# Kernel tuning notes

Hardware: AMD Instinct MI355X
Metric: run time of the kernel (lower is better)

## Reference

```python
import jax, jax.numpy as jnp
import numpy as np

STATE_DIM = 64
MEASURE_DIM = 32
N = 1048576  # measurement batch (broadcast column dim of z)


def setup_inputs() -> dict:
    key = jax.random.key(0)
    kz, kf = jax.random.split(key)
    z = jax.random.normal(kz, (MEASURE_DIM, N), dtype=jnp.float32)
    # Parameters initialized as in AKF.__init__ (identity matrices), with a
    # small perturbation on F so the dynamics are non-trivial but S stays
    # well-conditioned for the inverse.
    F = jnp.eye(STATE_DIM, dtype=jnp.float32) + 0.01 * jax.random.normal(kf, (STATE_DIM, STATE_DIM), dtype=jnp.float32)
    H = jnp.eye(MEASURE_DIM, STATE_DIM, dtype=jnp.float32)
    Q = jnp.eye(STATE_DIM, dtype=jnp.float32)
    R = jnp.eye(MEASURE_DIM, dtype=jnp.float32)
    P = jnp.eye(STATE_DIM, dtype=jnp.float32)
    x = jnp.zeros((STATE_DIM, 1), dtype=jnp.float32)
    return {"z": z, "F": F, "H": H, "Q": Q, "R": R, "P": P, "x": x}


def reference(z, F, H, Q, R, P, x):
    # One Kalman filter update step (predict + correct), batched over N
    # measurement columns in z. Returns the updated state estimate, matching
    # the torch module's `return self.x`.
    x_pred = F @ x                      # [s, 1]
    P_pred = F @ P @ F.T + Q            # [s, s]
    y = z - H @ x_pred                  # [m, N] (broadcast of [m,1])
    S = H @ P_pred @ H.T + R            # [m, m]
    K = P_pred @ H.T @ jnp.linalg.inv(S)  # [s, m]
    x_new = x_pred + K @ y              # [s, N]
    return x_new
```

## Files before the change

### kernel.cpp

```cpp
#include <hip/hip_runtime.h>

#define SD 64
#define MD 32

typedef float f32x4 __attribute__((ext_vector_type(4)));
typedef float f32x2 __attribute__((ext_vector_type(2)));

__device__ float g_Kb[SD * MD + SD];

__global__ __launch_bounds__(1024) void akf_prepare(
    const float* __restrict__ F, const float* __restrict__ H,
    const float* __restrict__ Q, const float* __restrict__ R,
    const float* __restrict__ P, const float* __restrict__ x)
{
    __shared__ __align__(16) float sF [SD * SD];
    __shared__ __align__(16) float sFt[SD * 68];
    __shared__ __align__(16) float sP [SD * SD];
    __shared__ __align__(16) float sT [SD * 68];
    __shared__ __align__(16) float sPp[SD * 68];
    __shared__ __align__(16) float sH [MD * SD];
    __shared__ __align__(16) float sHt[SD * 36];
    __shared__ __align__(16) float sA [SD * 36];
    __shared__ __align__(16) float sS [MD * 33];
    __shared__ __align__(16) float sSi[MD * 36];
    __shared__ __align__(16) float sK [SD * 36];
    __shared__ float sx[SD], sxp[SD], sHx[MD];

    const int tid = threadIdx.x;

    for (int idx = tid; idx < SD * SD; idx += 1024) {
        float f = F[idx], p = P[idx];
        int i = idx >> 6, j = idx & 63;
        sF[idx] = f;
        sFt[j * 68 + i] = f;
        sP[idx] = p;
    }
    for (int idx = tid; idx < MD * SD; idx += 1024) {
        float h = H[idx];
        int j = idx >> 6, k = idx & 63;
        sH[idx] = h;
        sHt[k * 36 + j] = h;
    }
    if (tid < SD) sx[tid] = x[tid];
    __syncthreads();

    if (tid < SD) {
        float a = 0.f;
        for (int k = 0; k < SD; ++k) a = fmaf(sFt[k * 68 + tid], sx[k], a);
        sxp[tid] = a;
    }

    {
        const int i = tid >> 4, j0 = (tid & 15) * 4;
        f32x4 acc = {0.f, 0.f, 0.f, 0.f};
        for (int k = 0; k < SD; ++k) {
            const float f = sF[i * 64 + k];
            const f32x4 p4 = *(const f32x4*)&sP[k * 64 + j0];
            acc.x = fmaf(f, p4.x, acc.x);
            acc.y = fmaf(f, p4.y, acc.y);
            acc.z = fmaf(f, p4.z, acc.z);
            acc.w = fmaf(f, p4.w, acc.w);
        }
        *(f32x4*)&sT[i * 68 + j0] = acc;
    }
    __syncthreads();

    {
        const int i = tid >> 4, j0 = (tid & 15) * 4;
        f32x4 acc = *(const f32x4*)&Q[i * 64 + j0];
        for (int k = 0; k < SD; ++k) {
            const float t = sT[i * 68 + k];
            const f32x4 f4 = *(const f32x4*)&sFt[k * 68 + j0];
            acc.x = fmaf(t, f4.x, acc.x);
            acc.y = fmaf(t, f4.y, acc.y);
            acc.z = fmaf(t, f4.z, acc.z);
            acc.w = fmaf(t, f4.w, acc.w);
        }
        *(f32x4*)&sPp[i * 68 + j0] = acc;
    }
    __syncthreads();

    if (tid < MD) {
        float a = 0.f;
        for (int k = 0; k < SD; ++k) a = fmaf(sHt[k * 36 + tid], sxp[k], a);
        sHx[tid] = a;
    }
    if (tid < 512) {
        const int i = tid >> 3, j0 = (tid & 7) * 4;
        f32x4 acc = {0.f, 0.f, 0.f, 0.f};
        for (int k = 0; k < SD; ++k) {
            const float p = sPp[i * 68 + k];
            const f32x4 h4 = *(const f32x4*)&sHt[k * 36 + j0];
            acc.x = fmaf(p, h4.x, acc.x);
            acc.y = fmaf(p, h4.y, acc.y);
            acc.z = fmaf(p, h4.z, acc.z);
            acc.w = fmaf(p, h4.w, acc.w);
        }
        *(f32x4*)&sA[i * 36 + j0] = acc;
    }
    __syncthreads();

    {
        const int i = tid >> 5, j = tid & 31;
        float a = R[i * 32 + j];
        for (int k = 0; k < SD; ++k) a = fmaf(sH[i * 64 + k], sA[k * 36 + j], a);
        sS[i * 33 + j] = a;
    }
    __syncthreads();

    if (tid < 64) {
        float col[MD];
#pragma unroll
        for (int i = 0; i < MD; ++i)
            col[i] = (tid < MD) ? sS[i * 33 + tid] : ((i == tid - MD) ? 1.f : 0.f);
#pragma unroll
        for (int kp = 0; kp < MD; ++kp) {
            const float piv = __shfl(col[kp], kp);
            const float r = 1.0f / piv;
            col[kp] *= r;
            const float pr = col[kp];
#pragma unroll
            for (int i = 0; i < MD; ++i) {
                if (i == kp) continue;
                const float f = __shfl(col[i], kp);
                col[i] = fmaf(-f, pr, col[i]);
            }
        }
        if (tid >= MD) {
            const int j = tid - MD;
#pragma unroll
            for (int i = 0; i < MD; ++i) sSi[i * 36 + j] = col[i];
        }
    }
    __syncthreads();

    if (tid < 512) {
        const int i = tid >> 3, j0 = (tid & 7) * 4;
        f32x4 acc = {0.f, 0.f, 0.f, 0.f};
        for (int k = 0; k < MD; ++k) {
            const float a = sA[i * 36 + k];
            const f32x4 s4 = *(const f32x4*)&sSi[k * 36 + j0];
            acc.x = fmaf(a, s4.x, acc.x);
            acc.y = fmaf(a, s4.y, acc.y);
            acc.z = fmaf(a, s4.z, acc.z);
            acc.w = fmaf(a, s4.w, acc.w);
        }
        *(f32x4*)&sK[i * 36 + j0] = acc;
        *(f32x4*)&g_Kb[i * MD + j0] = acc;
    }
    __syncthreads();

    if (tid < SD) {
        float a = sxp[tid];
        for (int j = 0; j < MD; ++j) a = fmaf(-sK[tid * 36 + j], sHx[j], a);
        g_Kb[SD * MD + tid] = a;
    }
}

__global__ __launch_bounds__(256) void akf_apply(
    const float* __restrict__ z, float* __restrict__ out, int N)
{
    const float* Kb = g_Kb;
    const int base = blockIdx.x * (256 * 8) + threadIdx.x * 4;

#pragma unroll 1
    for (int g = 0; g < 2; ++g) {
        const int c = base + g * (256 * 4);
        if (c >= N) continue;

        f32x4 zv[MD];
#pragma unroll
        for (int j = 0; j < MD; ++j)
            zv[j] = __builtin_nontemporal_load((const f32x4*)(z + (size_t)j * N + c));

#pragma unroll 4
        for (int i = 0; i < SD; ++i) {
            const float bi = Kb[SD * MD + i];
            f32x4 acc = {bi, bi, bi, bi};
#pragma unroll
            for (int j = 0; j < MD; ++j) {
                const float k = Kb[i * MD + j];
                acc.x = fmaf(k, zv[j].x, acc.x);
                acc.y = fmaf(k, zv[j].y, acc.y);
                acc.z = fmaf(k, zv[j].z, acc.z);
                acc.w = fmaf(k, zv[j].w, acc.w);
            }
            *(f32x4*)(out + (size_t)i * N + c) = acc;
        }
    }
}

extern "C" void kernel_launch(void* const* d_in, const int* in_sizes, int n_in,
                              void* d_out, int out_size, void* d_ws, size_t ws_size,
                              hipStream_t stream)
{
    const float* z = (const float*)d_in[0];
    const float* F = (const float*)d_in[1];
    const float* H = (const float*)d_in[2];
    const float* Q = (const float*)d_in[3];
    const float* R = (const float*)d_in[4];
    const float* P = (const float*)d_in[5];
    const float* x = (const float*)d_in[6];
    float* out = (float*)d_out;
    (void)d_ws; (void)ws_size;

    const int N = in_sizes[0] / MD;

    akf_prepare<<<1, 1024, 0, stream>>>(F, H, Q, R, P, x);

    const int cols_per_block = 256 * 8;
    const int nblocks = (N + cols_per_block - 1) / cols_per_block;
    akf_apply<<<nblocks, 256, 0, stream>>>(z, out, N);
}
```

Before: 403.2 us.

## Split output rows across waves and stream z rows with software prefetch

The apply kernel is restructured so each wave owns 16 of the 64 output rows for a 256-column tile. Each thread keeps 16 accumulators and streams z two rows at a time, prefetching the next pair. K is stored transposed so each wave reads contiguous row-blocks. The old design held all 32 z vectors in registers per thread. In the new one, the four waves of a block each load the same z columns, so z is read four times and relies on cache to absorb the extra traffic. The nontemporal z loads are also dropped, and register pressure and occupancy change.

```diff
diff --git a/kernel.cpp b/kernel.cpp
--- a/kernel.cpp
+++ b/kernel.cpp
@@ -6,7 +6,8 @@
 typedef float f32x4 __attribute__((ext_vector_type(4)));
 typedef float f32x2 __attribute__((ext_vector_type(2)));
 
-__device__ float g_Kb[SD * MD + SD];
+__device__ float g_Kt[MD * SD];
+__device__ float g_b[SD];
 
 __global__ __launch_bounds__(1024) void akf_prepare(
     const float* __restrict__ F, const float* __restrict__ H,
@@ -146,48 +147,73 @@
             acc.w = fmaf(a, s4.w, acc.w);
         }
         *(f32x4*)&sK[i * 36 + j0] = acc;
-        *(f32x4*)&g_Kb[i * MD + j0] = acc;
+        g_Kt[(j0 + 0) * SD + i] = acc.x;
+        g_Kt[(j0 + 1) * SD + i] = acc.y;
+        g_Kt[(j0 + 2) * SD + i] = acc.z;
+        g_Kt[(j0 + 3) * SD + i] = acc.w;
     }
     __syncthreads();
 
     if (tid < SD) {
         float a = sxp[tid];
         for (int j = 0; j < MD; ++j) a = fmaf(-sK[tid * 36 + j], sHx[j], a);
-        g_Kb[SD * MD + tid] = a;
+        g_b[tid] = a;
     }
 }
 
 __global__ __launch_bounds__(256) void akf_apply(
     const float* __restrict__ z, float* __restrict__ out, int N)
 {
-    const float* Kb = g_Kb;
-    const int base = blockIdx.x * (256 * 8) + threadIdx.x * 4;
+    const int lane = threadIdx.x & 63;
+    const int wave = threadIdx.x >> 6;
+    const int i0   = wave * 16;
+    const int c    = blockIdx.x * 256 + lane * 4;
+    if (c >= N) return;
+
+    f32x4 acc[16];
+#pragma unroll
+    for (int r = 0; r < 16; ++r) {
+        const float bi = g_b[i0 + r];
+        acc[r] = (f32x4){bi, bi, bi, bi};
+    }
+
+    const float* zc = z + c;
+    f32x4 zA = *(const f32x4*)(zc + (size_t)0 * N);
+    f32x4 zB = *(const f32x4*)(zc + (size_t)1 * N);
 
 #pragma unroll 1
-    for (int g = 0; g < 2; ++g) {
-        const int c = base + g * (256 * 4);
-        if (c >= N) continue;
-
-        f32x4 zv[MD];
-#pragma unroll
-        for (int j = 0; j < MD; ++j)
-            zv[j] = __builtin_nontemporal_load((const f32x4*)(z + (size_t)j * N + c));
-
-#pragma unroll 4
-        for (int i = 0; i < SD; ++i) {
-            const float bi = Kb[SD * MD + i];
-            f32x4 acc = {bi, bi, bi, bi};
-#pragma unroll
-            for (int j = 0; j < MD; ++j) {
-                const float k = Kb[i * MD + j];
-                acc.x = fmaf(k, zv[j].x, acc.x);
-                acc.y = fmaf(k, zv[j].y, acc.y);
-                acc.z = fmaf(k, zv[j].z, acc.z);
-                acc.w = fmaf(k, zv[j].w, acc.w);
-            }
-            *(f32x4*)(out + (size_t)i * N + c) = acc;
-        }
-    }
+    for (int j = 0; j < MD; j += 2) {
+        const int jn0 = (j + 2 < MD) ? j + 2 : MD - 2;
+        const int jn1 = (j + 3 < MD) ? j + 3 : MD - 1;
+        const f32x4 zC = *(const f32x4*)(zc + (size_t)jn0 * N);
+        const f32x4 zD = *(const f32x4*)(zc + (size_t)jn1 * N);
+
+        const float* kt0 = &g_Kt[(j + 0) * SD + i0];
+        const float* kt1 = &g_Kt[(j + 1) * SD + i0];
+#pragma unroll
+        for (int r = 0; r < 16; ++r) {
+            const float k0 = kt0[r];
+            acc[r].x = fmaf(k0, zA.x, acc[r].x);
+            acc[r].y = fmaf(k0, zA.y, acc[r].y);
+            acc[r].z = fmaf(k0, zA.z, acc[r].z);
+            acc[r].w = fmaf(k0, zA.w, acc[r].w);
+        }
+#pragma unroll
+        for (int r = 0; r < 16; ++r) {
+            const float k1 = kt1[r];
+            acc[r].x = fmaf(k1, zB.x, acc[r].x);
+            acc[r].y = fmaf(k1, zB.y, acc[r].y);
+            acc[r].z = fmaf(k1, zB.z, acc[r].z);
+            acc[r].w = fmaf(k1, zB.w, acc[r].w);
+        }
+        zA = zC;
+        zB = zD;
+    }
+
+    float* oc = out + c;
+#pragma unroll
+    for (int r = 0; r < 16; ++r)
+        *(f32x4*)(oc + (size_t)(i0 + r) * N) = acc[r];
 }
 
 extern "C" void kernel_launch(void* const* d_in, const int* in_sizes, int n_in,
@@ -208,7 +234,7 @@
 
     akf_prepare<<<1, 1024, 0, stream>>>(F, H, Q, R, P, x);
 
-    const int cols_per_block = 256 * 8;
+    const int cols_per_block = 256;
     const int nblocks = (N + cols_per_block - 1) / cols_per_block;
     akf_apply<<<nblocks, 256, 0, stream>>>(z, out, N);
 }
```

Result: slower. 487.9 us (+21.0%).

## Stage z tiles into LDS with async double-buffered loads in apply kernel

Applied to the files above, without the earlier changes.

Rewrites the batched K·z+b kernel to copy z tiles straight from global memory into shared memory with global_load_lds, double-buffered across four column tiles. Each wave computes 16 output rows from the shared tile, and K is stored transposed so its reads are uniform. The intent is to cut register pressure and overlap loads with compute and stores. The hand-tuned vmcnt wait counts are a correctness and ordering risk because outstanding stores also count toward vmcnt.

```diff
diff --git a/kernel.cpp b/kernel.cpp
--- a/kernel.cpp
+++ b/kernel.cpp
@@ -4,9 +4,9 @@
 #define MD 32
 
 typedef float f32x4 __attribute__((ext_vector_type(4)));
-typedef float f32x2 __attribute__((ext_vector_type(2)));
-
-__device__ float g_Kb[SD * MD + SD];
+
+__device__ float g_Kt[MD * SD];
+__device__ float g_b[SD];
 
 __global__ __launch_bounds__(1024) void akf_prepare(
     const float* __restrict__ F, const float* __restrict__ H,
@@ -146,46 +146,106 @@
             acc.w = fmaf(a, s4.w, acc.w);
         }
         *(f32x4*)&sK[i * 36 + j0] = acc;
-        *(f32x4*)&g_Kb[i * MD + j0] = acc;
+        g_Kt[(j0 + 0) * SD + i] = acc.x;
+        g_Kt[(j0 + 1) * SD + i] = acc.y;
+        g_Kt[(j0 + 2) * SD + i] = acc.z;
+        g_Kt[(j0 + 3) * SD + i] = acc.w;
     }
     __syncthreads();
 
     if (tid < SD) {
         float a = sxp[tid];
         for (int j = 0; j < MD; ++j) a = fmaf(-sK[tid * 36 + j], sHx[j], a);
-        g_Kb[SD * MD + tid] = a;
+        g_b[tid] = a;
     }
 }
+
+#define CT    256
+#define TILES 4
 
 __global__ __launch_bounds__(256) void akf_apply(
     const float* __restrict__ z, float* __restrict__ out, int N)
 {
-    const float* Kb = g_Kb;
-    const int base = blockIdx.x * (256 * 8) + threadIdx.x * 4;
-
-#pragma unroll 1
-    for (int g = 0; g < 2; ++g) {
-        const int c = base + g * (256 * 4);
-        if (c >= N) continue;
-
-        f32x4 zv[MD];
-#pragma unroll
-        for (int j = 0; j < MD; ++j)
-            zv[j] = __builtin_nontemporal_load((const f32x4*)(z + (size_t)j * N + c));
-
+    __shared__ __align__(16) float sZ[2][MD][CT];
+
+    const int lane = threadIdx.x & 63;
+    const int w    = threadIdx.x >> 6;
+    const int colb = lane * 4;
+    const int base = blockIdx.x * (CT * TILES);
+
+    if (base + CT * TILES <= N) {
+        auto stage = [&](int buf, int tc) {
+#pragma unroll
+            for (int k = 0; k < 8; ++k) {
+                const int j = w * 8 + k;
+                __builtin_amdgcn_global_load_lds(
+                    (const __attribute__((address_space(1))) unsigned int*)
+                        (z + (size_t)j * N + tc + colb),
+                    (__attribute__((address_space(3))) unsigned int*)
+                        &sZ[buf][j][0],
+                    16, 0, 0);
+            }
+        };
+
+        stage(0, base);
+
+#pragma unroll
+        for (int t = 0; t < TILES; ++t) {
+            const int buf = t & 1;
+            if (t + 1 < TILES) stage(buf ^ 1, base + (t + 1) * CT);
+
+            if (t == 0)
+                asm volatile("s_waitcnt vmcnt(8)" ::: "memory");
+            else if (t + 1 < TILES)
+                asm volatile("s_waitcnt vmcnt(24)" ::: "memory");
+            else
+                asm volatile("s_waitcnt vmcnt(16)" ::: "memory");
+            __builtin_amdgcn_s_barrier();
+            asm volatile("" ::: "memory");
+
+            const int tc = base + t * CT;
+#pragma unroll
+            for (int rg = 0; rg < 2; ++rg) {
+                const int i0 = w * 16 + rg * 8;
+                f32x4 acc[8];
+#pragma unroll
+                for (int r = 0; r < 8; ++r) {
+                    const float bi = g_b[i0 + r];
+                    acc[r] = (f32x4){bi, bi, bi, bi};
+                }
 #pragma unroll 4
-        for (int i = 0; i < SD; ++i) {
-            const float bi = Kb[SD * MD + i];
-            f32x4 acc = {bi, bi, bi, bi};
-#pragma unroll
-            for (int j = 0; j < MD; ++j) {
-                const float k = Kb[i * MD + j];
-                acc.x = fmaf(k, zv[j].x, acc.x);
-                acc.y = fmaf(k, zv[j].y, acc.y);
-                acc.z = fmaf(k, zv[j].z, acc.z);
-                acc.w = fmaf(k, zv[j].w, acc.w);
-            }
-            *(f32x4*)(out + (size_t)i * N + c) = acc;
+                for (int j = 0; j < MD; ++j) {
+                    const f32x4 zj = *(const f32x4*)&sZ[buf][j][colb];
+                    const float* kt = &g_Kt[j * SD + i0];
+#pragma unroll
+                    for (int r = 0; r < 8; ++r) {
+                        acc[r].x = fmaf(kt[r], zj.x, acc[r].x);
+                        acc[r].y = fmaf(kt[r], zj.y, acc[r].y);
+                        acc[r].z = fmaf(kt[r], zj.z, acc[r].z);
+                        acc[r].w = fmaf(kt[r], zj.w, acc[r].w);
+                    }
+                }
+#pragma unroll
+                for (int r = 0; r < 8; ++r)
+                    *(f32x4*)(out + (size_t)(i0 + r) * N + tc + colb) = acc[r];
+            }
+
+            asm volatile("s_waitcnt lgkmcnt(0)" ::: "memory");
+            __builtin_amdgcn_s_barrier();
+            asm volatile("" ::: "memory");
+        }
+    } else {
+        for (int c = base + (int)threadIdx.x; c < N; c += 256) {
+            float zc[MD];
+#pragma unroll
+            for (int j = 0; j < MD; ++j) zc[j] = z[(size_t)j * N + c];
+#pragma unroll 4
+            for (int i = 0; i < SD; ++i) {
+                float s = g_b[i];
+#pragma unroll
+                for (int j = 0; j < MD; ++j) s = fmaf(g_Kt[j * SD + i], zc[j], s);
+                out[(size_t)i * N + c] = s;
+            }
         }
     }
 }
@@ -208,7 +268,7 @@
 
     akf_prepare<<<1, 1024, 0, stream>>>(F, H, Q, R, P, x);
 
-    const int cols_per_block = 256 * 8;
+    const int cols_per_block = CT * TILES;
     const int nblocks = (N + cols_per_block - 1) / cols_per_block;
     akf_apply<<<nblocks, 256, 0, stream>>>(z, out, N);
 }
```

Result: slower. 449.2 us (+11.4%).
